# Performance work log

Hardware: AMD Instinct MI355X
Metric: run time of the kernel (lower is better)

The kernel has to match this reference:

```python
import jax, jax.numpy as jnp
import numpy as np

N_ATOMS = 100000
N_PAIRS = 3200000
N_PROP = 16
N_BASIS = 10
W = 16  # MLP width for pp/pi/ii nodes


def setup_inputs() -> dict:
    key = jax.random.key(0)
    ks = jax.random.split(key, 16)
    s = 0.1
    inp = {
        "ind_2": jax.random.randint(ks[0], (N_PAIRS, 2), 0, N_ATOMS),
        "p1": jax.random.normal(ks[1], (N_ATOMS, N_PROP), dtype=jnp.float32),
        "basis": jax.random.normal(ks[2], (N_PAIRS, N_BASIS), dtype=jnp.float32),
        # pp_pre: [16,16], bias=True
        "Wpre0": jax.random.normal(ks[3], (N_PROP, W), dtype=jnp.float32) * s,
        "bpre0": jnp.zeros((W,), dtype=jnp.float32),
        "Wpre1": jax.random.normal(ks[4], (W, W), dtype=jnp.float32) * s,
        "bpre1": jnp.zeros((W,), dtype=jnp.float32),
        # pi: input 2*W -> W -> W*n_basis, bias=True
        "Wpi0": jax.random.normal(ks[5], (2 * W, W), dtype=jnp.float32) * s,
        "bpi0": jnp.zeros((W,), dtype=jnp.float32),
        "Wpi1": jax.random.normal(ks[6], (W, W * N_BASIS), dtype=jnp.float32) * s,
        "bpi1": jnp.zeros((W * N_BASIS,), dtype=jnp.float32),
        # ii: [16,16], bias=False
        "Wii0": jax.random.normal(ks[7], (W, W), dtype=jnp.float32) * s,
        "Wii1": jax.random.normal(ks[8], (W, W), dtype=jnp.float32) * s,
        # pp_post: [16,16], bias=False
        "Wpost0": jax.random.normal(ks[9], (W, W), dtype=jnp.float32) * s,
        "Wpost1": jax.random.normal(ks[10], (W, W), dtype=jnp.float32) * s,
    }
    return inp


def reference(ind_2, p1, basis, Wpre0, bpre0, Wpre1, bpre1,
              Wpi0, bpi0, Wpi1, bpi1, Wii0, Wii1, Wpost0, Wpost1):
    act = jnp.tanh
    n_atoms = p1.shape[0]
    # pp_pre: per-atom FF (activation on every dense, bias=True)
    p1_in = act(p1 @ Wpre0 + bpre0)
    p1_in = act(p1_in @ Wpre1 + bpre1)
    # PI: gather pair endpoints, concat, MLP, contract with radial basis
    h = jnp.concatenate([p1_in[ind_2[:, 0]], p1_in[ind_2[:, 1]]], axis=-1)  # (P, 2W)
    h = act(h @ Wpi0 + bpi0)                                                # (P, W)
    h = act(h @ Wpi1 + bpi1)                                                # (P, W*n_basis)
    h = h.reshape(h.shape[0], -1, basis.shape[-1])                          # (P, W, n_basis)
    i_pair = jnp.einsum('pcb,pb->pc', h, basis)                             # (P, W)
    # II: pair-mixing FF (bias=False)
    i_pair = act(i_pair @ Wii0)
    i_pair = act(i_pair @ Wii1)
    # IP: scatter-sum pair features back to atoms at ind_2[:,0]
    p_sum = jax.ops.segment_sum(i_pair, ind_2[:, 0], num_segments=n_atoms)  # (A, W)
    # pp_post (bias=False)
    p1_new = act(p_sum @ Wpost0)
    p1_new = act(p1_new @ Wpost1)
    return (p1_new, i_pair)
```

## Files before the change

kernel.cpp:

```cpp
#include <hip/hip_runtime.h>

#define N_ATOMS 100000
#define N_PAIRS 3200000
#define N_PROP 16
#define N_BASIS 10
#define W 16
#define NSUP (N_PAIRS / 32)
#define SCAN_BLK 1024
#define NB ((N_ATOMS + SCAN_BLK - 1) / SCAN_BLK)
#define SC 2.88539008177792681f

typedef short  s16x8 __attribute__((ext_vector_type(8)));
typedef float  f32x4 __attribute__((ext_vector_type(4)));

__device__ __forceinline__ float tanh_pre(float y) {
    float e = __builtin_amdgcn_exp2f(y);
    return 1.0f - 2.0f * __builtin_amdgcn_rcpf(e + 1.0f);
}
__device__ __forceinline__ float fast_tanh(float x) {
    float e = __builtin_amdgcn_exp2f(x * SC);
    return 1.0f - 2.0f * __builtin_amdgcn_rcpf(e + 1.0f);
}
__device__ __forceinline__ unsigned short bf16r(float f) {
    union { float f; unsigned u; } v; v.f = f;
    unsigned r = v.u + 0x7FFFu + ((v.u >> 16) & 1u);
    return (unsigned short)(r >> 16);
}
__device__ __forceinline__ unsigned cvt_pk_bf16(float a, float b) {
    unsigned r;
    asm("v_cvt_pk_bf16_f32 %0, %1, %2" : "=v"(r) : "v"(a), "v"(b));
    return r;
}
__device__ __forceinline__ float bitf(unsigned u) {
    union { unsigned u; float f; } v; v.u = u; return v.f;
}

__global__ __launch_bounds__(256) void k_pp_pre(
    const float* __restrict__ p1,
    const float* __restrict__ W0, const float* __restrict__ b0,
    const float* __restrict__ W1, const float* __restrict__ b1,
    const float* __restrict__ Wpi0, const float* __restrict__ bpi0,
    float* __restrict__ ytop, float* __restrict__ ybot)
{
    int a = blockIdx.x * 256 + threadIdx.x;
    if (a >= N_ATOMS) return;
    const float4* src = reinterpret_cast<const float4*>(p1 + (size_t)a * N_PROP);
    float4 v0 = src[0], v1 = src[1], v2 = src[2], v3 = src[3];
    float x[N_PROP] = {v0.x,v0.y,v0.z,v0.w, v1.x,v1.y,v1.z,v1.w,
                       v2.x,v2.y,v2.z,v2.w, v3.x,v3.y,v3.z,v3.w};
    float h[W];
#pragma unroll
    for (int c = 0; c < W; ++c) h[c] = b0[c];
#pragma unroll
    for (int k = 0; k < N_PROP; ++k)
#pragma unroll
        for (int c = 0; c < W; ++c) h[c] += x[k] * W0[k*W + c];
#pragma unroll
    for (int c = 0; c < W; ++c) h[c] = fast_tanh(h[c]);
    float y[W];
#pragma unroll
    for (int c = 0; c < W; ++c) y[c] = b1[c];
#pragma unroll
    for (int k = 0; k < W; ++k)
#pragma unroll
        for (int c = 0; c < W; ++c) y[c] += h[k] * W1[k*W + c];
    float t[W];
#pragma unroll
    for (int c = 0; c < W; ++c) t[c] = fast_tanh(y[c]);

    float yt[W], yb[W];
#pragma unroll
    for (int c = 0; c < W; ++c) { yt[c] = bpi0[c]; yb[c] = 0.0f; }
#pragma unroll
    for (int k = 0; k < W; ++k)
#pragma unroll
        for (int c = 0; c < W; ++c) {
            yt[c] += t[k] * Wpi0[k*W + c];
            yb[c] += t[k] * Wpi0[(W + k)*W + c];
        }
    float4* dt = reinterpret_cast<float4*>(ytop + (size_t)a * W);
    float4* db = reinterpret_cast<float4*>(ybot + (size_t)a * W);
#pragma unroll
    for (int q = 0; q < 4; ++q) {
        dt[q] = make_float4(SC*yt[4*q], SC*yt[4*q+1], SC*yt[4*q+2], SC*yt[4*q+3]);
        db[q] = make_float4(SC*yb[4*q], SC*yb[4*q+1], SC*yb[4*q+2], SC*yb[4*q+3]);
    }
}

__device__ __forceinline__ void make_B_hilo(const float x[4], int idxA, int idxB,
                                            int g, bool augment, s16x8& Bh, s16x8& Bl)
{
    unsigned w0h = cvt_pk_bf16(x[0], x[1]);
    unsigned w1h = cvt_pk_bf16(x[2], x[3]);
    float f0 = bitf(w0h << 16), f1 = bitf(w0h & 0xFFFF0000u);
    float f2 = bitf(w1h << 16), f3 = bitf(w1h & 0xFFFF0000u);
    unsigned w0l = cvt_pk_bf16(x[0] - f0, x[1] - f1);
    unsigned w1l = cvt_pk_bf16(x[2] - f2, x[3] - f3);
    union { unsigned u[4]; s16x8 v; } H, L;
    H.u[0] = (unsigned)__shfl((int)w0h, idxA); H.u[1] = (unsigned)__shfl((int)w1h, idxA);
    H.u[2] = (unsigned)__shfl((int)w0h, idxB); H.u[3] = (unsigned)__shfl((int)w1h, idxB);
    L.u[0] = (unsigned)__shfl((int)w0l, idxA); L.u[1] = (unsigned)__shfl((int)w1l, idxA);
    L.u[2] = (unsigned)__shfl((int)w0l, idxB); L.u[3] = (unsigned)__shfl((int)w1l, idxB);
    if (augment && g == 2) { H.u[0] = 0x3F80u; L.u[0] = 0u; }
    Bh = H.v; Bl = L.v;
}

__device__ __forceinline__ s16x8 make_B_hi(const float x[4], int idxA, int idxB)
{
    unsigned w0 = cvt_pk_bf16(x[0], x[1]);
    unsigned w1 = cvt_pk_bf16(x[2], x[3]);
    union { unsigned u[4]; s16x8 v; } H;
    H.u[0] = (unsigned)__shfl((int)w0, idxA); H.u[1] = (unsigned)__shfl((int)w1, idxA);
    H.u[2] = (unsigned)__shfl((int)w0, idxB); H.u[3] = (unsigned)__shfl((int)w1, idxB);
    return H.v;
}

template<int USE_RANK>
__global__ __launch_bounds__(256) void k_pair_mfma(
    const int*   __restrict__ ind2,
    const float* __restrict__ basis,
    const float* __restrict__ ytop,
    const float* __restrict__ ybot,
    const float* __restrict__ Wpi1, const float* __restrict__ bpi1,
    const float* __restrict__ Wii0, const float* __restrict__ Wii1,
    float* __restrict__ i_pair_out,
    const unsigned* __restrict__ starts,
    const unsigned* __restrict__ rank,
    unsigned* __restrict__ cursor,
    float* __restrict__ svals)
{
    __shared__ s16x8 a2_lds[12][4][16];

    const int lane = threadIdx.x & 63;
    const int w    = threadIdx.x >> 6;
    const int r    = lane & 15;
    const int g    = lane >> 4;
    const int idxA = (r + 32*g) & 63;
    const int idxB = (idxA + 16) & 63;
    const int2* ind2v = reinterpret_cast<const int2*>(ind2);

    for (int e = threadIdx.x; e < 768; e += 256) {
        int t  = e >> 6;
        int rr = (e >> 2) & 15;
        int gg = e & 3;
        int ch = 4*(rr >> 2) + (t & 3);
        int bp = 4*(t >> 2) + (rr & 3);
        s16x8 val;
#pragma unroll
        for (int j = 0; j < 8; ++j) {
            int k = 8*gg + j;
            float wv = 0.0f;
            if (bp < N_BASIS) {
                if (k < W)       wv = Wpi1[k*(W*N_BASIS) + ch*N_BASIS + bp];
                else if (k == W) wv = bpi1[ch*N_BASIS + bp];
            }
            val[j] = (short)bf16r(SC * wv);
        }
        a2_lds[t][gg][rr] = val;
    }

    s16x8 a3, a4;
#pragma unroll
    for (int j = 0; j < 8; ++j) {
        int k = 8*g + j;
        a3[j] = (short)(k < W ? bf16r(SC * Wii0[k*W + r]) : 0);
        a4[j] = (short)(k < W ? bf16r(SC * Wii1[k*W + r]) : 0);
    }

    __syncthreads();

    const int stride = gridDim.x * 4;
    int sup = blockIdx.x * 4 + w;
    if (sup >= NSUP) return;

    int2 ijA = ind2v[(size_t)sup * 32 + r];
    int2 ijB = ind2v[(size_t)sup * 32 + r + 16];
    f32x4 ytA = *reinterpret_cast<const f32x4*>(ytop + (size_t)ijA.x * W + 4*g);
    f32x4 ybA = *reinterpret_cast<const f32x4*>(ybot + (size_t)ijA.y * W + 4*g);
    f32x4 ytB = *reinterpret_cast<const f32x4*>(ytop + (size_t)ijB.x * W + 4*g);
    f32x4 ybB = *reinterpret_cast<const f32x4*>(ybot + (size_t)ijB.y * W + 4*g);

    for (; sup < NSUP; sup += stride) {
        const int pA = sup * 32 + r;
        const int pB = pA + 16;
        const int nsupc = (sup + stride < NSUP) ? (sup + stride) : sup;

        int2 nijA = ind2v[(size_t)nsupc * 32 + r];
        int2 nijB = ind2v[(size_t)nsupc * 32 + r + 16];

        float h0A[4], h0B[4];
#pragma unroll
        for (int i = 0; i < 4; ++i) {
            h0A[i] = tanh_pre(ytA[i] + ybA[i]);
            h0B[i] = tanh_pre(ytB[i] + ybB[i]);
        }
        s16x8 B2hA, B2lA, B2hB, B2lB;
        make_B_hilo(h0A, idxA, idxB, g, true, B2hA, B2lA);
        make_B_hilo(h0B, idxA, idxB, g, true, B2hB, B2lB);

        float basA[N_BASIS], basB[N_BASIS];
        {
            const float2* bbA = reinterpret_cast<const float2*>(basis + (size_t)pA * N_BASIS);
            const float2* bbB = reinterpret_cast<const float2*>(basis + (size_t)pB * N_BASIS);
#pragma unroll
            for (int q = 0; q < 5; ++q) {
                float2 tA = bbA[q]; basA[2*q] = tA.x; basA[2*q+1] = tA.y;
                float2 tB = bbB[q]; basB[2*q] = tB.x; basB[2*q+1] = tB.y;
            }
        }

        float vlA[4] = {0.f,0.f,0.f,0.f}, vlB[4] = {0.f,0.f,0.f,0.f};
#pragma unroll
        for (int t = 0; t < 12; ++t) {
            s16x8 af = a2_lds[t][g][r];
            f32x4 zA = {0.f,0.f,0.f,0.f}, zB = {0.f,0.f,0.f,0.f};
            zA = __builtin_amdgcn_mfma_f32_16x16x32_bf16(af, B2hA, zA, 0, 0, 0);
            zB = __builtin_amdgcn_mfma_f32_16x16x32_bf16(af, B2hB, zB, 0, 0, 0);
            zA = __builtin_amdgcn_mfma_f32_16x16x32_bf16(af, B2lA, zA, 0, 0, 0);
            zB = __builtin_amdgcn_mfma_f32_16x16x32_bf16(af, B2lB, zB, 0, 0, 0);
#pragma unroll
            for (int i = 0; i < 4; ++i) {
                const int bi = 4*(t >> 2) + i;
                if (bi < N_BASIS) {
                    const int m = t & 3;
                    vlA[m] += tanh_pre(zA[i]) * basA[bi];
                    vlB[m] += tanh_pre(zB[i]) * basB[bi];
                }
            }
        }

        f32x4 nytA = *reinterpret_cast<const f32x4*>(ytop + (size_t)nijA.x * W + 4*g);
        f32x4 nybA = *reinterpret_cast<const f32x4*>(ybot + (size_t)nijA.y * W + 4*g);
        f32x4 nytB = *reinterpret_cast<const f32x4*>(ytop + (size_t)nijB.x * W + 4*g);
        f32x4 nybB = *reinterpret_cast<const f32x4*>(ybot + (size_t)nijB.y * W + 4*g);

        s16x8 B3hA = make_B_hi(vlA, idxA, idxB);
        s16x8 B3hB = make_B_hi(vlB, idxA, idxB);
        f32x4 uaA = {0.f,0.f,0.f,0.f}, uaB = {0.f,0.f,0.f,0.f};
        uaA = __builtin_amdgcn_mfma_f32_16x16x32_bf16(a3, B3hA, uaA, 0, 0, 0);
        uaB = __builtin_amdgcn_mfma_f32_16x16x32_bf16(a3, B3hB, uaB, 0, 0, 0);
        float tuA[4], tuB[4];
#pragma unroll
        for (int i = 0; i < 4; ++i) {
            tuA[i] = tanh_pre(uaA[i]);
            tuB[i] = tanh_pre(uaB[i]);
        }

        s16x8 B4hA = make_B_hi(tuA, idxA, idxB);
        s16x8 B4hB = make_B_hi(tuB, idxA, idxB);
        f32x4 waA = {0.f,0.f,0.f,0.f}, waB = {0.f,0.f,0.f,0.f};
        waA = __builtin_amdgcn_mfma_f32_16x16x32_bf16(a4, B4hA, waA, 0, 0, 0);
        waB = __builtin_amdgcn_mfma_f32_16x16x32_bf16(a4, B4hB, waB, 0, 0, 0);
        float4 outA = make_float4(tanh_pre(waA[0]), tanh_pre(waA[1]),
                                  tanh_pre(waA[2]), tanh_pre(waA[3]));
        float4 outB = make_float4(tanh_pre(waB[0]), tanh_pre(waB[1]),
                                  tanh_pre(waB[2]), tanh_pre(waB[3]));

        *reinterpret_cast<float4*>(i_pair_out + (size_t)pA * W + 4*g) = outA;
        *reinterpret_cast<float4*>(i_pair_out + (size_t)pB * W + 4*g) = outB;

        unsigned posA, posB;
        if (USE_RANK) {
            posA = starts[ijA.x] + rank[pA];
            posB = starts[ijB.x] + rank[pB];
        } else {
            unsigned ppA = 0, ppB = 0;
            if (g == 0) {
                ppA = atomicAdd(&cursor[ijA.x], 1u);
                ppB = atomicAdd(&cursor[ijB.x], 1u);
            }
            posA = (unsigned)__shfl((int)ppA, r);
            posB = (unsigned)__shfl((int)ppB, r);
        }
        *reinterpret_cast<float4*>(svals + (size_t)posA * W + 4*g) = outA;
        *reinterpret_cast<float4*>(svals + (size_t)posB * W + 4*g) = outB;

        ijA = nijA; ijB = nijB;
        ytA = nytA; ybA = nybA; ytB = nytB; ybB = nybB;
    }
}

__global__ __launch_bounds__(256) void k_count(const int* __restrict__ ind2,
                                               unsigned* __restrict__ counts,
                                               unsigned* __restrict__ rank)
{
    int p = blockIdx.x * 256 + threadIdx.x;
    if (p >= N_PAIRS) return;
    rank[p] = atomicAdd(&counts[ind2[2*p]], 1u);
}

__global__ __launch_bounds__(SCAN_BLK) void k_scanA(const unsigned* __restrict__ counts,
                                                    unsigned* __restrict__ starts,
                                                    unsigned* __restrict__ bsum)
{
    __shared__ unsigned sc[SCAN_BLK];
    int a = blockIdx.x * SCAN_BLK + threadIdx.x;
    unsigned c = (a < N_ATOMS) ? counts[a] : 0u;
    sc[threadIdx.x] = c;
    __syncthreads();
    for (int off = 1; off < SCAN_BLK; off <<= 1) {
        unsigned v = sc[threadIdx.x];
        unsigned add = (threadIdx.x >= off) ? sc[threadIdx.x - off] : 0u;
        __syncthreads();
        sc[threadIdx.x] = v + add;
        __syncthreads();
    }
    if (a < N_ATOMS) starts[a] = sc[threadIdx.x] - c;
    if (threadIdx.x == SCAN_BLK - 1) bsum[blockIdx.x] = sc[SCAN_BLK - 1];
}

__global__ __launch_bounds__(128) void k_scanB(const unsigned* __restrict__ bsum,
                                               unsigned* __restrict__ boff)
{
    __shared__ unsigned s[128];
    int t = threadIdx.x;
    unsigned v = (t < NB) ? bsum[t] : 0u;
    s[t] = v;
    __syncthreads();
    for (int off = 1; off < 128; off <<= 1) {
        unsigned x = s[t];
        unsigned add = (t >= off) ? s[t - off] : 0u;
        __syncthreads();
        s[t] = x + add;
        __syncthreads();
    }
    if (t < NB) boff[t] = s[t] - v;
}

__global__ __launch_bounds__(SCAN_BLK) void k_scanC(unsigned* __restrict__ starts,
                                                    const unsigned* __restrict__ boff,
                                                    unsigned* __restrict__ cursor)
{
    int a = blockIdx.x * SCAN_BLK + threadIdx.x;
    if (a >= N_ATOMS) return;
    unsigned s = starts[a] + boff[blockIdx.x];
    starts[a] = s;
    cursor[a] = s;
}

__global__ __launch_bounds__(256) void k_reduce_stream(const unsigned* __restrict__ starts,
                                                       const unsigned* __restrict__ counts,
                                                       const float* __restrict__ svals,
                                                       float* __restrict__ p_sum)
{
    int a = blockIdx.x * 4 + (threadIdx.x >> 6);
    if (a >= N_ATOMS) return;
    int lane = threadIdx.x & 63;
    int c = lane & 15, q = lane >> 4;
    unsigned n = counts[a], st = starts[a];
    float acc = 0.0f;
    for (unsigned k = q; k < n; k += 4)
        acc += svals[(size_t)(st + k) * W + c];
    acc += __shfl_xor(acc, 16);
    acc += __shfl_xor(acc, 32);
    if (q == 0) p_sum[(size_t)a * W + c] = acc;
}

__global__ __launch_bounds__(256) void k_pp_post(
    const float* __restrict__ p_sum,
    const float* __restrict__ W0, const float* __restrict__ W1,
    float* __restrict__ p1_new)
{
    int a = blockIdx.x * 256 + threadIdx.x;
    if (a >= N_ATOMS) return;
    const float4* src = reinterpret_cast<const float4*>(p_sum + (size_t)a * W);
    float4 v0 = src[0], v1 = src[1], v2 = src[2], v3 = src[3];
    float x[W] = {v0.x,v0.y,v0.z,v0.w, v1.x,v1.y,v1.z,v1.w,
                  v2.x,v2.y,v2.z,v2.w, v3.x,v3.y,v3.z,v3.w};
    float h[W];
#pragma unroll
    for (int c = 0; c < W; ++c) h[c] = 0.0f;
#pragma unroll
    for (int k = 0; k < W; ++k)
#pragma unroll
        for (int c = 0; c < W; ++c) h[c] += x[k] * W0[k*W + c];
#pragma unroll
    for (int c = 0; c < W; ++c) h[c] = fast_tanh(h[c]);
    float y[W];
#pragma unroll
    for (int c = 0; c < W; ++c) y[c] = 0.0f;
#pragma unroll
    for (int k = 0; k < W; ++k)
#pragma unroll
        for (int c = 0; c < W; ++c) y[c] += h[k] * W1[k*W + c];
    float4* dst = reinterpret_cast<float4*>(p1_new + (size_t)a * W);
    dst[0] = make_float4(fast_tanh(y[0]),  fast_tanh(y[1]),  fast_tanh(y[2]),  fast_tanh(y[3]));
    dst[1] = make_float4(fast_tanh(y[4]),  fast_tanh(y[5]),  fast_tanh(y[6]),  fast_tanh(y[7]));
    dst[2] = make_float4(fast_tanh(y[8]),  fast_tanh(y[9]),  fast_tanh(y[10]), fast_tanh(y[11]));
    dst[3] = make_float4(fast_tanh(y[12]), fast_tanh(y[13]), fast_tanh(y[14]), fast_tanh(y[15]));
}

extern "C" void kernel_launch(void* const* d_in, const int* in_sizes, int n_in,
                              void* d_out, int out_size, void* d_ws, size_t ws_size,
                              hipStream_t stream) {
    const int*   ind2   = (const int*)d_in[0];
    const float* p1     = (const float*)d_in[1];
    const float* basis  = (const float*)d_in[2];
    const float* Wpre0  = (const float*)d_in[3];
    const float* bpre0  = (const float*)d_in[4];
    const float* Wpre1  = (const float*)d_in[5];
    const float* bpre1  = (const float*)d_in[6];
    const float* Wpi0   = (const float*)d_in[7];
    const float* bpi0   = (const float*)d_in[8];
    const float* Wpi1   = (const float*)d_in[9];
    const float* bpi1   = (const float*)d_in[10];
    const float* Wii0   = (const float*)d_in[11];
    const float* Wii1   = (const float*)d_in[12];
    const float* Wpost0 = (const float*)d_in[13];
    const float* Wpost1 = (const float*)d_in[14];

    float* out    = (float*)d_out;
    float* p1_new = out;
    float* i_pair = out + (size_t)N_ATOMS * W;

    char* ws = (char*)d_ws;
    float*    ytop   = (float*)ws;                                ws += (size_t)N_ATOMS * W * 4;
    float*    ybot   = (float*)ws;                                ws += (size_t)N_ATOMS * W * 4;
    float*    p_sum  = (float*)ws;                                ws += (size_t)N_ATOMS * W * 4;
    unsigned* counts = (unsigned*)ws;                             ws += (size_t)N_ATOMS * 4;
    unsigned* starts = (unsigned*)ws;                             ws += (size_t)N_ATOMS * 4;
    unsigned* cursor = (unsigned*)ws;                             ws += (size_t)N_ATOMS * 4;
    unsigned* bsum   = (unsigned*)ws;                             ws += 1024 * 4;
    unsigned* boff   = (unsigned*)ws;                             ws += 1024 * 4;
    float*    svals  = (float*)ws;                                ws += (size_t)N_PAIRS * W * 4;
    unsigned* rank   = (unsigned*)ws;                             ws += (size_t)N_PAIRS * 4;

    int use_rank = (ws_size >= (size_t)(ws - (char*)d_ws));

    hipMemsetAsync(counts, 0, (size_t)N_ATOMS * sizeof(unsigned), stream);
    k_pp_pre<<<(N_ATOMS + 255) / 256, 256, 0, stream>>>(p1, Wpre0, bpre0, Wpre1, bpre1,
                                                        Wpi0, bpi0, ytop, ybot);
    k_count<<<(N_PAIRS + 255) / 256, 256, 0, stream>>>(ind2, counts, use_rank ? rank : cursor);
    k_scanA<<<NB, SCAN_BLK, 0, stream>>>(counts, starts, bsum);
    k_scanB<<<1, 128, 0, stream>>>(bsum, boff);
    k_scanC<<<NB, SCAN_BLK, 0, stream>>>(starts, boff, cursor);

    if (use_rank) {
        k_pair_mfma<1><<<2560, 256, 0, stream>>>(ind2, basis, ytop, ybot,
                                                 Wpi1, bpi1, Wii0, Wii1,
                                                 i_pair, starts, rank, cursor, svals);
    } else {
        k_pair_mfma<0><<<2560, 256, 0, stream>>>(ind2, basis, ytop, ybot,
                                                 Wpi1, bpi1, Wii0, Wii1,
                                                 i_pair, starts, rank, cursor, svals);
    }
    k_reduce_stream<<<(N_ATOMS + 3) / 4, 256, 0, stream>>>(starts, counts, svals, p_sum);
    k_pp_post<<<(N_ATOMS + 255) / 256, 256, 0, stream>>>(p_sum, Wpost0, Wpost1, p1_new);
}
```

Before: 559.0 us.

## Switch pair MLP to 32x32x16 MFMA layout with non-temporal output stores

```diff
diff --git a/kernel.cpp b/kernel.cpp
--- a/kernel.cpp
+++ b/kernel.cpp
@@ -10,8 +10,9 @@
 #define NB ((N_ATOMS + SCAN_BLK - 1) / SCAN_BLK)
 #define SC 2.88539008177792681f
 
-typedef short  s16x8 __attribute__((ext_vector_type(8)));
-typedef float  f32x4 __attribute__((ext_vector_type(4)));
+typedef short  s16x8  __attribute__((ext_vector_type(8)));
+typedef float  f32x4  __attribute__((ext_vector_type(4)));
+typedef float  f32x16 __attribute__((ext_vector_type(16)));
 
 __device__ __forceinline__ float tanh_pre(float y) {
     float e = __builtin_amdgcn_exp2f(y);
@@ -33,6 +34,10 @@
 }
 __device__ __forceinline__ float bitf(unsigned u) {
     union { unsigned u; float f; } v; v.u = u; return v.f;
+}
+__device__ __forceinline__ void nt_store4(float* p, float a, float b, float c, float d) {
+    f32x4 v = {a, b, c, d};
+    __builtin_nontemporal_store(v, reinterpret_cast<f32x4*>(p));
 }
 
 __global__ __launch_bounds__(256) void k_pp_pre(
@@ -85,34 +90,6 @@
         dt[q] = make_float4(SC*yt[4*q], SC*yt[4*q+1], SC*yt[4*q+2], SC*yt[4*q+3]);
         db[q] = make_float4(SC*yb[4*q], SC*yb[4*q+1], SC*yb[4*q+2], SC*yb[4*q+3]);
     }
-}
-
-__device__ __forceinline__ void make_B_hilo(const float x[4], int idxA, int idxB,
-                                            int g, bool augment, s16x8& Bh, s16x8& Bl)
-{
-    unsigned w0h = cvt_pk_bf16(x[0], x[1]);
-    unsigned w1h = cvt_pk_bf16(x[2], x[3]);
-    float f0 = bitf(w0h << 16), f1 = bitf(w0h & 0xFFFF0000u);
-    float f2 = bitf(w1h << 16), f3 = bitf(w1h & 0xFFFF0000u);
-    unsigned w0l = cvt_pk_bf16(x[0] - f0, x[1] - f1);
-    unsigned w1l = cvt_pk_bf16(x[2] - f2, x[3] - f3);
-    union { unsigned u[4]; s16x8 v; } H, L;
-    H.u[0] = (unsigned)__shfl((int)w0h, idxA); H.u[1] = (unsigned)__shfl((int)w1h, idxA);
-    H.u[2] = (unsigned)__shfl((int)w0h, idxB); H.u[3] = (unsigned)__shfl((int)w1h, idxB);
-    L.u[0] = (unsigned)__shfl((int)w0l, idxA); L.u[1] = (unsigned)__shfl((int)w1l, idxA);
-    L.u[2] = (unsigned)__shfl((int)w0l, idxB); L.u[3] = (unsigned)__shfl((int)w1l, idxB);
-    if (augment && g == 2) { H.u[0] = 0x3F80u; L.u[0] = 0u; }
-    Bh = H.v; Bl = L.v;
-}
-
-__device__ __forceinline__ s16x8 make_B_hi(const float x[4], int idxA, int idxB)
-{
-    unsigned w0 = cvt_pk_bf16(x[0], x[1]);
-    unsigned w1 = cvt_pk_bf16(x[2], x[3]);
-    union { unsigned u[4]; s16x8 v; } H;
-    H.u[0] = (unsigned)__shfl((int)w0, idxA); H.u[1] = (unsigned)__shfl((int)w1, idxA);
-    H.u[2] = (unsigned)__shfl((int)w0, idxB); H.u[3] = (unsigned)__shfl((int)w1, idxB);
-    return H.v;
 }
 
 template<int USE_RANK>
@@ -129,154 +106,176 @@
     unsigned* __restrict__ cursor,
     float* __restrict__ svals)
 {
-    __shared__ s16x8 a2_lds[12][4][16];
+    __shared__ s16x8 aw_lds[5][2][32];
+    __shared__ s16x8 ab_lds[5][2][32];
 
     const int lane = threadIdx.x & 63;
-    const int w    = threadIdx.x >> 6;
-    const int r    = lane & 15;
-    const int g    = lane >> 4;
-    const int idxA = (r + 32*g) & 63;
-    const int idxB = (idxA + 16) & 63;
+    const int wv   = threadIdx.x >> 6;
+    const int col  = lane & 31;
+    const int h    = lane >> 5;
+
+    for (int e = threadIdx.x; e < 320; e += 256) {
+        int T = e >> 6, hh = (e >> 5) & 1, row = e & 31;
+        int colW = (4*(row >> 3) + (row & 3)) * N_BASIS + 2*T + ((row >> 2) & 1);
+        s16x8 wfrag, bfrag;
+#pragma unroll
+        for (int j = 0; j < 8; ++j) {
+            int k = 8*hh + j;
+            wfrag[j] = (short)bf16r(SC * Wpi1[k*(W*N_BASIS) + colW]);
+            bfrag[j] = (short)((k == 0) ? bf16r(SC * bpi1[colW]) : 0);
+        }
+        aw_lds[T][hh][row] = wfrag;
+        ab_lds[T][hh][row] = bfrag;
+    }
+
+    s16x8 a3, a4;
+#pragma unroll
+    for (int j = 0; j < 8; ++j) {
+        int k = 8*h + j;
+        a3[j] = (short)(col < W ? bf16r(SC * Wii0[k*W + col]) : 0);
+        a4[j] = (short)(col < W ? bf16r(SC * Wii1[k*W + col]) : 0);
+    }
+    s16x8 Bones = {0,0,0,0,0,0,0,0};
+    if (h == 0) Bones[0] = (short)0x3F80;
+
+    __syncthreads();
+
+    const int stride = gridDim.x * 4;
+    int sup = blockIdx.x * 4 + wv;
+    if (sup >= NSUP) return;
     const int2* ind2v = reinterpret_cast<const int2*>(ind2);
 
-    for (int e = threadIdx.x; e < 768; e += 256) {
-        int t  = e >> 6;
-        int rr = (e >> 2) & 15;
-        int gg = e & 3;
-        int ch = 4*(rr >> 2) + (t & 3);
-        int bp = 4*(t >> 2) + (rr & 3);
-        s16x8 val;
-#pragma unroll
-        for (int j = 0; j < 8; ++j) {
-            int k = 8*gg + j;
-            float wv = 0.0f;
-            if (bp < N_BASIS) {
-                if (k < W)       wv = Wpi1[k*(W*N_BASIS) + ch*N_BASIS + bp];
-                else if (k == W) wv = bpi1[ch*N_BASIS + bp];
-            }
-            val[j] = (short)bf16r(SC * wv);
-        }
-        a2_lds[t][gg][rr] = val;
-    }
-
-    s16x8 a3, a4;
-#pragma unroll
-    for (int j = 0; j < 8; ++j) {
-        int k = 8*g + j;
-        a3[j] = (short)(k < W ? bf16r(SC * Wii0[k*W + r]) : 0);
-        a4[j] = (short)(k < W ? bf16r(SC * Wii1[k*W + r]) : 0);
-    }
-
-    __syncthreads();
-
-    const int stride = gridDim.x * 4;
-    int sup = blockIdx.x * 4 + w;
-    if (sup >= NSUP) return;
-
-    int2 ijA = ind2v[(size_t)sup * 32 + r];
-    int2 ijB = ind2v[(size_t)sup * 32 + r + 16];
-    f32x4 ytA = *reinterpret_cast<const f32x4*>(ytop + (size_t)ijA.x * W + 4*g);
-    f32x4 ybA = *reinterpret_cast<const f32x4*>(ybot + (size_t)ijA.y * W + 4*g);
-    f32x4 ytB = *reinterpret_cast<const f32x4*>(ytop + (size_t)ijB.x * W + 4*g);
-    f32x4 ybB = *reinterpret_cast<const f32x4*>(ybot + (size_t)ijB.y * W + 4*g);
+    int2 ij = ind2v[(size_t)sup * 32 + col];
+    f32x4 yt0 = *reinterpret_cast<const f32x4*>(ytop + (size_t)ij.x * W + 8*h);
+    f32x4 yt1 = *reinterpret_cast<const f32x4*>(ytop + (size_t)ij.x * W + 8*h + 4);
+    f32x4 yb0 = *reinterpret_cast<const f32x4*>(ybot + (size_t)ij.y * W + 8*h);
+    f32x4 yb1 = *reinterpret_cast<const f32x4*>(ybot + (size_t)ij.y * W + 8*h + 4);
 
     for (; sup < NSUP; sup += stride) {
-        const int pA = sup * 32 + r;
-        const int pB = pA + 16;
-        const int nsupc = (sup + stride < NSUP) ? (sup + stride) : sup;
-
-        int2 nijA = ind2v[(size_t)nsupc * 32 + r];
-        int2 nijB = ind2v[(size_t)nsupc * 32 + r + 16];
-
-        float h0A[4], h0B[4];
-#pragma unroll
-        for (int i = 0; i < 4; ++i) {
-            h0A[i] = tanh_pre(ytA[i] + ybA[i]);
-            h0B[i] = tanh_pre(ytB[i] + ybB[i]);
-        }
-        s16x8 B2hA, B2lA, B2hB, B2lB;
-        make_B_hilo(h0A, idxA, idxB, g, true, B2hA, B2lA);
-        make_B_hilo(h0B, idxA, idxB, g, true, B2hB, B2lB);
-
-        float basA[N_BASIS], basB[N_BASIS];
-        {
-            const float2* bbA = reinterpret_cast<const float2*>(basis + (size_t)pA * N_BASIS);
-            const float2* bbB = reinterpret_cast<const float2*>(basis + (size_t)pB * N_BASIS);
-#pragma unroll
-            for (int q = 0; q < 5; ++q) {
-                float2 tA = bbA[q]; basA[2*q] = tA.x; basA[2*q+1] = tA.y;
-                float2 tB = bbB[q]; basB[2*q] = tB.x; basB[2*q+1] = tB.y;
-            }
-        }
-
-        float vlA[4] = {0.f,0.f,0.f,0.f}, vlB[4] = {0.f,0.f,0.f,0.f};
-#pragma unroll
-        for (int t = 0; t < 12; ++t) {
-            s16x8 af = a2_lds[t][g][r];
-            f32x4 zA = {0.f,0.f,0.f,0.f}, zB = {0.f,0.f,0.f,0.f};
-            zA = __builtin_amdgcn_mfma_f32_16x16x32_bf16(af, B2hA, zA, 0, 0, 0);
-            zB = __builtin_amdgcn_mfma_f32_16x16x32_bf16(af, B2hB, zB, 0, 0, 0);
-            zA = __builtin_amdgcn_mfma_f32_16x16x32_bf16(af, B2lA, zA, 0, 0, 0);
-            zB = __builtin_amdgcn_mfma_f32_16x16x32_bf16(af, B2lB, zB, 0, 0, 0);
-#pragma unroll
-            for (int i = 0; i < 4; ++i) {
-                const int bi = 4*(t >> 2) + i;
-                if (bi < N_BASIS) {
-                    const int m = t & 3;
-                    vlA[m] += tanh_pre(zA[i]) * basA[bi];
-                    vlB[m] += tanh_pre(zB[i]) * basB[bi];
-                }
-            }
-        }
-
-        f32x4 nytA = *reinterpret_cast<const f32x4*>(ytop + (size_t)nijA.x * W + 4*g);
-        f32x4 nybA = *reinterpret_cast<const f32x4*>(ybot + (size_t)nijA.y * W + 4*g);
-        f32x4 nytB = *reinterpret_cast<const f32x4*>(ytop + (size_t)nijB.x * W + 4*g);
-        f32x4 nybB = *reinterpret_cast<const f32x4*>(ybot + (size_t)nijB.y * W + 4*g);
-
-        s16x8 B3hA = make_B_hi(vlA, idxA, idxB);
-        s16x8 B3hB = make_B_hi(vlB, idxA, idxB);
-        f32x4 uaA = {0.f,0.f,0.f,0.f}, uaB = {0.f,0.f,0.f,0.f};
-        uaA = __builtin_amdgcn_mfma_f32_16x16x32_bf16(a3, B3hA, uaA, 0, 0, 0);
-        uaB = __builtin_amdgcn_mfma_f32_16x16x32_bf16(a3, B3hB, uaB, 0, 0, 0);
-        float tuA[4], tuB[4];
-#pragma unroll
-        for (int i = 0; i < 4; ++i) {
-            tuA[i] = tanh_pre(uaA[i]);
-            tuB[i] = tanh_pre(uaB[i]);
-        }
-
-        s16x8 B4hA = make_B_hi(tuA, idxA, idxB);
-        s16x8 B4hB = make_B_hi(tuB, idxA, idxB);
-        f32x4 waA = {0.f,0.f,0.f,0.f}, waB = {0.f,0.f,0.f,0.f};
-        waA = __builtin_amdgcn_mfma_f32_16x16x32_bf16(a4, B4hA, waA, 0, 0, 0);
-        waB = __builtin_amdgcn_mfma_f32_16x16x32_bf16(a4, B4hB, waB, 0, 0, 0);
-        float4 outA = make_float4(tanh_pre(waA[0]), tanh_pre(waA[1]),
-                                  tanh_pre(waA[2]), tanh_pre(waA[3]));
-        float4 outB = make_float4(tanh_pre(waB[0]), tanh_pre(waB[1]),
-                                  tanh_pre(waB[2]), tanh_pre(waB[3]));
-
-        *reinterpret_cast<float4*>(i_pair_out + (size_t)pA * W + 4*g) = outA;
-        *reinterpret_cast<float4*>(i_pair_out + (size_t)pB * W + 4*g) = outB;
-
-        unsigned posA, posB;
+        const int p = sup * 32 + col;
+        const int nsup = (sup + stride < NSUP) ? (sup + stride) : sup;
+
+        int2 nij = ind2v[(size_t)nsup * 32 + col];
+
+        float h0[8];
+#pragma unroll
+        for (int j = 0; j < 4; ++j) h0[j]     = tanh_pre(yt0[j] + yb0[j]);
+#pragma unroll
+        for (int j = 0; j < 4; ++j) h0[4 + j] = tanh_pre(yt1[j] + yb1[j]);
+        unsigned w0h = cvt_pk_bf16(h0[0], h0[1]);
+        unsigned w1h = cvt_pk_bf16(h0[2], h0[3]);
+        unsigned w2h = cvt_pk_bf16(h0[4], h0[5]);
+        unsigned w3h = cvt_pk_bf16(h0[6], h0[7]);
+        unsigned w0l = cvt_pk_bf16(h0[0] - bitf(w0h << 16), h0[1] - bitf(w0h & 0xFFFF0000u));
+        unsigned w1l = cvt_pk_bf16(h0[2] - bitf(w1h << 16), h0[3] - bitf(w1h & 0xFFFF0000u));
+        unsigned w2l = cvt_pk_bf16(h0[4] - bitf(w2h << 16), h0[5] - bitf(w2h & 0xFFFF0000u));
+        unsigned w3l = cvt_pk_bf16(h0[6] - bitf(w3h << 16), h0[7] - bitf(w3h & 0xFFFF0000u));
+        union { unsigned u[4]; s16x8 v; } BH, BL;
+        BH.u[0] = w0h; BH.u[1] = w1h; BH.u[2] = w2h; BH.u[3] = w3h;
+        BL.u[0] = w0l; BL.u[1] = w1l; BL.u[2] = w2l; BL.u[3] = w3l;
+        s16x8 B2h = BH.v, B2l = BL.v;
+
+        const float2* bb = reinterpret_cast<const float2*>(basis + (size_t)p * N_BASIS);
+        float bsel[5];
+#pragma unroll
+        for (int q = 0; q < 5; ++q) {
+            float2 t2 = bb[q];
+            bsel[q] = h ? t2.y : t2.x;
+        }
+
+        float v[16];
+#pragma unroll
+        for (int i = 0; i < 16; ++i) v[i] = 0.0f;
+#pragma unroll
+        for (int T = 0; T < 5; ++T) {
+            s16x8 af = aw_lds[T][h][col];
+            s16x8 ab = ab_lds[T][h][col];
+            f32x16 z = {0.0f};
+            z = __builtin_amdgcn_mfma_f32_32x32x16_bf16(ab, Bones, z, 0, 0, 0);
+            z = __builtin_amdgcn_mfma_f32_32x32x16_bf16(af, B2h,  z, 0, 0, 0);
+            z = __builtin_amdgcn_mfma_f32_32x32x16_bf16(af, B2l,  z, 0, 0, 0);
+#pragma unroll
+            for (int i = 0; i < 16; ++i)
+                v[i] += tanh_pre(z[i]) * bsel[T];
+        }
+
+        f32x4 nyt0 = *reinterpret_cast<const f32x4*>(ytop + (size_t)nij.x * W + 8*h);
+        f32x4 nyt1 = *reinterpret_cast<const f32x4*>(ytop + (size_t)nij.x * W + 8*h + 4);
+        f32x4 nyb0 = *reinterpret_cast<const f32x4*>(ybot + (size_t)nij.y * W + 8*h);
+        f32x4 nyb1 = *reinterpret_cast<const f32x4*>(ybot + (size_t)nij.y * W + 8*h + 4);
+
+        float own[8], snd[8];
+        if (h == 0) {
+#pragma unroll
+            for (int j = 0; j < 8; ++j) { own[j] = v[j]; snd[j] = v[8 + j]; }
+        } else {
+#pragma unroll
+            for (int j = 0; j < 8; ++j) { own[j] = v[8 + j]; snd[j] = v[j]; }
+        }
+        float vf[8];
+#pragma unroll
+        for (int j = 0; j < 8; ++j) vf[j] = own[j] + __shfl_xor(snd[j], 32);
+
+        union { unsigned u[4]; s16x8 v; } B3u;
+        B3u.u[0] = cvt_pk_bf16(vf[0], vf[1]);
+        B3u.u[1] = cvt_pk_bf16(vf[2], vf[3]);
+        B3u.u[2] = cvt_pk_bf16(vf[4], vf[5]);
+        B3u.u[3] = cvt_pk_bf16(vf[6], vf[7]);
+        f32x16 ua = {0.0f};
+        ua = __builtin_amdgcn_mfma_f32_32x32x16_bf16(a3, B3u.v, ua, 0, 0, 0);
+        float u[8];
+#pragma unroll
+        for (int i = 0; i < 8; ++i) u[i] = tanh_pre(ua[i]);
+
+        float uo[4], us[4];
+        if (h == 0) {
+#pragma unroll
+            for (int j = 0; j < 4; ++j) { uo[j] = u[j]; us[j] = u[4 + j]; }
+        } else {
+#pragma unroll
+            for (int j = 0; j < 4; ++j) { uo[j] = u[4 + j]; us[j] = u[j]; }
+        }
+        float ur[4];
+#pragma unroll
+        for (int j = 0; j < 4; ++j) ur[j] = __shfl_xor(us[j], 32);
+        union { unsigned u[4]; s16x8 v; } B4u;
+        if (h == 0) {
+            B4u.u[0] = cvt_pk_bf16(uo[0], uo[1]);
+            B4u.u[1] = cvt_pk_bf16(uo[2], uo[3]);
+            B4u.u[2] = cvt_pk_bf16(ur[0], ur[1]);
+            B4u.u[3] = cvt_pk_bf16(ur[2], ur[3]);
+        } else {
+            B4u.u[0] = cvt_pk_bf16(ur[0], ur[1]);
+            B4u.u[1] = cvt_pk_bf16(ur[2], ur[3]);
+            B4u.u[2] = cvt_pk_bf16(uo[0], uo[1]);
+            B4u.u[3] = cvt_pk_bf16(uo[2], uo[3]);
+        }
+        f32x16 wa = {0.0f};
+        wa = __builtin_amdgcn_mfma_f32_32x32x16_bf16(a4, B4u.v, wa, 0, 0, 0);
+        float wq[8];
+#pragma unroll
+        for (int i = 0; i < 8; ++i) wq[i] = tanh_pre(wa[i]);
+
+        const int off1 = h ? 4 : 0;
+        const int off2 = h ? 12 : 8;
+        float* ob = i_pair_out + (size_t)p * W;
+        nt_store4(ob + off1, wq[0], wq[1], wq[2], wq[3]);
+        nt_store4(ob + off2, wq[4], wq[5], wq[6], wq[7]);
+
+        unsigned pos;
         if (USE_RANK) {
-            posA = starts[ijA.x] + rank[pA];
-            posB = starts[ijB.x] + rank[pB];
+            pos = starts[ij.x] + rank[p];
         } else {
-            unsigned ppA = 0, ppB = 0;
-            if (g == 0) {
-                ppA = atomicAdd(&cursor[ijA.x], 1u);
-                ppB = atomicAdd(&cursor[ijB.x], 1u);
-            }
-            posA = (unsigned)__shfl((int)ppA, r);
-            posB = (unsigned)__shfl((int)ppB, r);
-        }
-        *reinterpret_cast<float4*>(svals + (size_t)posA * W + 4*g) = outA;
-        *reinterpret_cast<float4*>(svals + (size_t)posB * W + 4*g) = outB;
-
-        ijA = nijA; ijB = nijB;
-        ytA = nytA; ybA = nybA; ytB = nytB; ybB = nybB;
+            unsigned pp = 0;
+            if (h == 0) pp = atomicAdd(&cursor[ij.x], 1u);
+            pos = (unsigned)__shfl((int)pp, col);
+        }
+        float* sb = svals + (size_t)pos * W;
+        nt_store4(sb + off1, wq[0], wq[1], wq[2], wq[3]);
+        nt_store4(sb + off2, wq[4], wq[5], wq[6], wq[7]);
+
+        ij = nij;
+        yt0 = nyt0; yt1 = nyt1; yb0 = nyb0; yb1 = nyb1;
     }
 }
 
```

Result: no change. 548.4 us (-1.9%).
